# Kernel tuning notes

Measured on AMD Instinct MI355X. Metric: run time of the kernel, lower is better.

## Reference

```python
import jax, jax.numpy as jnp
import numpy as np

B, S, E, H, D = 4, 2048, 1024, 16, 64  # batch, seq, embed, heads, head_dim


def setup_inputs() -> dict:
    key = jax.random.key(0)
    k1, k2, k3 = jax.random.split(key, 3)
    x = jax.random.normal(k1, (B, S, E), dtype=jnp.float32)
    qkv_w = jax.random.normal(k2, (E, H, 3 * D), dtype=jnp.float32) * (1.0 / np.sqrt(E))
    qkv_b = jnp.zeros((H, 3 * D), dtype=jnp.float32)
    out_w = jax.random.normal(k3, (H, D, E), dtype=jnp.float32) * (1.0 / np.sqrt(H * D))
    out_b = jnp.zeros((E,), dtype=jnp.float32)
    return {"x": x, "qkv_w": qkv_w, "qkv_b": qkv_b, "out_w": out_w, "out_b": out_b}


def _large_negative_number(dtype):
    return jnp.asarray(-0.7 * jnp.finfo(dtype).max, dtype=dtype)


def reference(x, qkv_w, qkv_b, out_w, out_b):
    # qkv projection: LinearGeneral(E -> (H, 3D))
    qkv = jnp.einsum('bse,ehd->bshd', x, qkv_w) + qkv_b  # [B,S,H,3D]
    q, k, v = jnp.split(qkv, 3, axis=-1)  # each [B,S,H,D]
    logits = jnp.einsum('bqhd,bkhd->bhqk', q, k)  # [B,H,S,S]
    logits = logits / jnp.sqrt(jnp.asarray(q.shape[-1], logits.dtype))
    mask = jnp.tril(jnp.ones((q.shape[1], q.shape[1]), dtype=jnp.bool_))
    logits = jnp.where(mask, logits, _large_negative_number(logits.dtype))
    probs = jax.nn.softmax(logits, axis=-1)
    attn = jnp.einsum('bhqk,bkhd->bqhd', probs, v)  # [B,S,H,D]
    # output projection: LinearGeneral((H, D) -> E)
    return jnp.einsum('bqhd,hde->bqe', attn, out_w) + out_b
```

## Files before the change

### kernel.cpp

```cpp
#include <hip/hip_runtime.h>

typedef unsigned int u32;
typedef _Float16 f16;
typedef _Float16 f16x8 __attribute__((ext_vector_type(8)));
typedef _Float16 f16x4 __attribute__((ext_vector_type(4)));
typedef float f32x4 __attribute__((ext_vector_type(4)));

#define LOG2E 1.4426950408889634f

__device__ __forceinline__ void gl_lds16(const void* g, void* l) {
  __builtin_amdgcn_global_load_lds(
      (const __attribute__((address_space(1))) u32*)g,
      (__attribute__((address_space(3))) u32*)l, 16, 0, 0);
}

__device__ __forceinline__ f32x4 mfma16(f16x8 a, f16x8 b, f32x4 c) {
  return __builtin_amdgcn_mfma_f32_16x16x32_f16(a, b, c, 0, 0, 0);
}

__global__ void k_cvt(const float* __restrict__ in, f16* __restrict__ out, int n4) {
  int stride = gridDim.x * blockDim.x;
  for (int i = blockIdx.x * blockDim.x + threadIdx.x; i < n4; i += stride) {
    f32x4 v = *(const f32x4*)(in + (size_t)i * 4);
    f16x4 o;
    o[0] = (f16)v[0]; o[1] = (f16)v[1]; o[2] = (f16)v[2]; o[3] = (f16)v[3];
    *(f16x4*)(out + (size_t)i * 4) = o;
  }
}

__global__ void k_tconv(const float* __restrict__ in, f16* __restrict__ out, int R, int C) {
  __shared__ f16 tile[32][33];
  int c0 = blockIdx.x * 32, r0 = blockIdx.y * 32;
  int tx = threadIdx.x, ty = threadIdx.y;
#pragma unroll
  for (int i = ty; i < 32; i += 8)
    tile[i][tx] = (f16)in[(size_t)(r0 + i) * C + c0 + tx];
  __syncthreads();
#pragma unroll
  for (int i = ty; i < 32; i += 8)
    out[(size_t)(c0 + i) * R + r0 + tx] = tile[tx][i];
}


__device__ __forceinline__ void gemm_core(
    const f16* __restrict__ A, const f16* __restrict__ Bt,
    int bm, int bn, f16* SM, int w, int lane, f32x4 (&acc)[4][4]) {
  constexpr int KT = 16;
  const int g = lane >> 4, rl = lane & 15;
  const int l4 = lane >> 2, ls = lane & 3;
  const int wr = w >> 1, wc = w & 1;

  const int cr0 = w * 32 + l4, cr1 = cr0 + 16, br = w * 16 + l4;
  const f16* aS0 = A + (size_t)(bm + cr0) * 1024 + ((ls ^ ((cr0 >> 1) & 3)) * 8);
  const f16* aS1 = A + (size_t)(bm + cr1) * 1024 + ((ls ^ ((cr1 >> 1) & 3)) * 8);
  const f16* bS  = Bt + (size_t)(bn + br) * 1024 + ((ls ^ ((br >> 1) & 3)) * 8);

#define STG_A(b, ks, kt) do { \
    gl_lds16(aS0 + (kt) * 64 + (ks) * 32, SM + (b) * 16384 + (ks) * 8192 + (w * 2 + 0) * 512); \
    gl_lds16(aS1 + (kt) * 64 + (ks) * 32, SM + (b) * 16384 + (ks) * 8192 + (w * 2 + 1) * 512); } while (0)
#define STG_B(b, ks, kt) \
    gl_lds16(bS + (kt) * 64 + (ks) * 32, SM + 49152 + (b) * 8192 + (ks) * 4096 + w * 512)

  STG_A(0, 0, 0); STG_B(0, 0, 0); STG_A(0, 1, 0); STG_B(0, 1, 0);
  STG_A(1, 0, 1); STG_B(1, 0, 1); STG_A(1, 1, 1); STG_B(1, 1, 1);
  asm volatile("s_waitcnt vmcnt(6)" ::: "memory");
  __builtin_amdgcn_s_barrier();

  int c = 0, cs = 2;
#pragma unroll 1
  for (int kt = 0; kt < KT; ++kt) {
    const f16* Ab = SM + c * 16384;
    const f16* Bb = SM + 49152 + c * 8192;
    const bool stg = (kt + 2 < KT);
    f16x8 bf[4][2];

    {
#pragma unroll
      for (int j = 0; j < 4; ++j)
#pragma unroll
        for (int ks = 0; ks < 2; ++ks) {
          const int rb = wc * 64 + j * 16 + rl;
          bf[j][ks] = *(const f16x8*)(Bb + ks * 4096 + rb * 32 + ((g ^ ((rb >> 1) & 3)) * 8));
        }
      f16x8 af[2][2];
#pragma unroll
      for (int mi = 0; mi < 2; ++mi)
#pragma unroll
        for (int ks = 0; ks < 2; ++ks) {
          const int ra = wr * 64 + mi * 16 + rl;
          af[mi][ks] = *(const f16x8*)(Ab + ks * 8192 + ra * 32 + ((g ^ ((ra >> 1) & 3)) * 8));
        }
      if (stg) { STG_A(cs, 0, kt + 2); STG_B(cs, 0, kt + 2); }
      __builtin_amdgcn_s_barrier();
      asm volatile("s_waitcnt lgkmcnt(0)" ::: "memory");
      __builtin_amdgcn_sched_barrier(0);
      __builtin_amdgcn_s_setprio(1);
#pragma unroll
      for (int mi = 0; mi < 2; ++mi)
#pragma unroll
        for (int j = 0; j < 4; ++j) {
          acc[mi][j] = mfma16(af[mi][0], bf[j][0], acc[mi][j]);
          acc[mi][j] = mfma16(af[mi][1], bf[j][1], acc[mi][j]);
        }
      __builtin_amdgcn_s_setprio(0);
      __builtin_amdgcn_sched_barrier(0);
      __builtin_amdgcn_s_barrier();
    }

    {
      f16x8 af[2][2];
#pragma unroll
      for (int mi = 0; mi < 2; ++mi)
#pragma unroll
        for (int ks = 0; ks < 2; ++ks) {
          const int ra = wr * 64 + (2 + mi) * 16 + rl;
          af[mi][ks] = *(const f16x8*)(Ab + ks * 8192 + ra * 32 + ((g ^ ((ra >> 1) & 3)) * 8));
        }
      if (stg) { STG_A(cs, 1, kt + 2); STG_B(cs, 1, kt + 2); }
      __builtin_amdgcn_s_barrier();
      asm volatile("s_waitcnt lgkmcnt(0)" ::: "memory");
      __builtin_amdgcn_sched_barrier(0);
      __builtin_amdgcn_s_setprio(1);
#pragma unroll
      for (int mi = 0; mi < 2; ++mi)
#pragma unroll
        for (int j = 0; j < 4; ++j) {
          acc[2 + mi][j] = mfma16(af[mi][0], bf[j][0], acc[2 + mi][j]);
          acc[2 + mi][j] = mfma16(af[mi][1], bf[j][1], acc[2 + mi][j]);
        }
      __builtin_amdgcn_s_setprio(0);
      __builtin_amdgcn_sched_barrier(0);
      if (kt + 2 < KT)      { asm volatile("s_waitcnt vmcnt(6)" ::: "memory"); }
      else if (kt + 1 < KT) { asm volatile("s_waitcnt vmcnt(0)" ::: "memory"); }
      __builtin_amdgcn_s_barrier();
    }

    c = (c == 2) ? 0 : c + 1;
    cs = (cs == 2) ? 0 : cs + 1;
  }
#undef STG_A
#undef STG_B
}

__global__ __launch_bounds__(512, 2) void k_gemm_qkv3(
    const f16* __restrict__ A, const f16* __restrict__ Bt,
    const float* __restrict__ bias,
    f16* __restrict__ qo, f16* __restrict__ ko2, f16* __restrict__ vto) {
  __shared__ __align__(16) f16 SM[73728];
  const int lin0 = blockIdx.y * 24 + blockIdx.x;
  const int lin = (lin0 & 7) * 96 + (lin0 >> 3);
  const int bn = (lin % 24) * 128, bm = (lin / 24) * 256;
  const int t = threadIdx.x, lane = t & 63, w = t >> 6;
  const int g = lane >> 4, rl = lane & 15;
  const int wr = w >> 1, wc = w & 1;

  f32x4 acc[4][4] = {};
  gemm_core(A, Bt, bm, bn, SM, w, lane, acc);

#pragma unroll
  for (int i = 0; i < 4; ++i)
#pragma unroll
    for (int j = 0; j < 4; ++j)
#pragma unroll
      for (int r = 0; r < 4; ++r) {
        int m = bm + wr * 64 + i * 16 + g * 4 + r;
        int n = bn + wc * 64 + j * 16 + rl;
        float v = acc[i][j][r] + bias[n];
        int b = m >> 11, s = m & 2047;
        int h = n / 192, rem = n - h * 192;
        int tsel = rem >> 6, d = rem & 63;
        size_t bh = (size_t)(b * 16 + h);
        if (tsel == 0)      qo[(bh * 2048 + s) * 64 + d] = (f16)(v * (0.125f * LOG2E));
        else if (tsel == 1) ko2[(bh * 2048 + s) * 64 + d] = (f16)v;
        else                vto[(bh * 64 + d) * 2048 + s] = (f16)v;
      }
}

__global__ __launch_bounds__(512, 2) void k_gemm_out3(
    const f16* __restrict__ A, const f16* __restrict__ Bt,
    const float* __restrict__ bias, float* __restrict__ out) {
  __shared__ __align__(16) f16 SM[73728];
  const int lin0 = blockIdx.y * 8 + blockIdx.x;
  const int lin = (lin0 & 7) * 32 + (lin0 >> 3);
  const int bn = (lin % 8) * 128, bm = (lin / 8) * 256;
  const int t = threadIdx.x, lane = t & 63, w = t >> 6;
  const int g = lane >> 4, rl = lane & 15;
  const int wr = w >> 1, wc = w & 1;

  f32x4 acc[4][4] = {};
  gemm_core(A, Bt, bm, bn, SM, w, lane, acc);

#pragma unroll
  for (int i = 0; i < 4; ++i)
#pragma unroll
    for (int j = 0; j < 4; ++j)
#pragma unroll
      for (int r = 0; r < 4; ++r) {
        int m = bm + wr * 64 + i * 16 + g * 4 + r;
        int n = bn + wc * 64 + j * 16 + rl;
        out[(size_t)m * 1024 + n] = acc[i][j][r] + bias[n];
      }
}

__global__ __launch_bounds__(256, 4) void k_attn2(
    const f16* __restrict__ q, const f16* __restrict__ kgl,
    const f16* __restrict__ vt, f16* __restrict__ o) {
  constexpr int S = 2048;
  __shared__ __align__(16) f16 Ks[2][64 * 64];
  __shared__ __align__(16) f16 Vs[2][64 * 64];
  __shared__ __align__(16) f16 Ps[4][16 * 64];

  const int blk = blockIdx.x;
  const int sidx = blk >> 3;
  const int bh = (blk & 7) * 8 + (sidx & 7);
  const int qb = 15 - (sidx >> 3);

  const int t = threadIdx.x, lane = t & 63, w = t >> 6;
  const int g = lane >> 4, rl = lane & 15;

  const f16* qp = q + ((size_t)bh * S + qb * 128) * 64;
  const f16* kb = kgl + (size_t)bh * S * 64;
  const f16* vb = vt + (size_t)bh * 64 * S;

  f16x8 qf[2][2];
#pragma unroll
  for (int sub = 0; sub < 2; ++sub)
#pragma unroll
    for (int ks = 0; ks < 2; ++ks)
      qf[sub][ks] = *(const f16x8*)(qp + (size_t)(w * 32 + sub * 16 + rl) * 64 + ks * 32 + g * 8);

  f32x4 oacc[2][4] = {};
  float lrow[2] = {0.f, 0.f};

  const int srow = lane >> 3;
  const int sslot = (lane & 7) ^ srow;

  const int nkt = 2 * qb + 2;
  const int qmaxw = qb * 128 + w * 32 + 31;

  auto STAGE = [&](int bufi, int kt) {
#pragma unroll
    for (int i = 0; i < 2; ++i) {
      const int r0 = w * 16 + i * 8;
      gl_lds16(kb + (size_t)(kt * 64 + r0 + srow) * 64 + sslot * 8, &Ks[bufi][r0 * 64]);
      gl_lds16(vb + (size_t)(r0 + srow) * S + kt * 64 + sslot * 8, &Vs[bufi][r0 * 64]);
    }
  };

  STAGE(0, 0);
  __syncthreads();
  int buf = 0;

  for (int kt = 0; kt < nkt; ++kt) {
    if (kt + 1 < nkt) STAGE(buf ^ 1, kt + 1);

    if (kt * 64 <= qmaxw) {
      const f16* Kb = &Ks[buf][0];
      const f16* Vb = &Vs[buf][0];
#pragma unroll
      for (int sub = 0; sub < 2; ++sub) {
        const int qsub = qb * 128 + w * 32 + sub * 16;
        if (kt * 64 > qsub + 15) continue;

        f32x4 sT[4] = {};
#pragma unroll
        for (int j = 0; j < 4; ++j)
#pragma unroll
          for (int ks = 0; ks < 2; ++ks) {
            int row = j * 16 + rl;
            f16x8 kf = *(const f16x8*)(Kb + row * 64 + (((ks * 4 + g) ^ (rl & 7)) * 8));
            sT[j] = mfma16(kf, qf[sub][ks], sT[j]);
          }

        if (kt * 64 + 63 > qsub) {
#pragma unroll
          for (int j = 0; j < 4; ++j)
#pragma unroll
            for (int r = 0; r < 4; ++r)
              if (kt * 64 + j * 16 + g * 4 + r > qsub + rl) sT[j][r] = -1e30f;
        }

        float ps = 0.f;
#pragma unroll
        for (int j = 0; j < 4; ++j) {
          f16x4 pb;
#pragma unroll
          for (int r = 0; r < 4; ++r) {
            float p = exp2f(sT[j][r]);
            ps += p;
            pb[r] = (f16)p;
          }
          *(f16x4*)(&Ps[w][0] + rl * 64 + (((j * 2 + (g >> 1)) ^ (rl & 7)) * 8) + (g & 1) * 4) = pb;
        }
        lrow[sub] += ps;

        asm volatile("s_waitcnt lgkmcnt(0)" ::: "memory");
        __builtin_amdgcn_sched_barrier(0);

        f16x8 pf[2];
#pragma unroll
        for (int ks = 0; ks < 2; ++ks)
          pf[ks] = *(const f16x8*)(&Ps[w][0] + rl * 64 + (((ks * 4 + g) ^ (rl & 7)) * 8));

#pragma unroll
        for (int dj = 0; dj < 4; ++dj)
#pragma unroll
          for (int ks = 0; ks < 2; ++ks) {
            int vrow = dj * 16 + rl;
            f16x8 vf = *(const f16x8*)(Vb + vrow * 64 + (((ks * 4 + g) ^ (rl & 7)) * 8));
            oacc[sub][dj] = mfma16(pf[ks], vf, oacc[sub][dj]);
          }
      }
    }
    __syncthreads();
    buf ^= 1;
  }

  float rinv[2];
#pragma unroll
  for (int sub = 0; sub < 2; ++sub) {
    float s_ = lrow[sub];
    s_ += __shfl_xor(s_, 16, 64);
    s_ += __shfl_xor(s_, 32, 64);
    rinv[sub] = 1.0f / s_;
  }

  const int h = bh & 15;
  const size_t rowb = (size_t)(bh >> 4) * 2048 + qb * 128 + w * 32;
#pragma unroll
  for (int sub = 0; sub < 2; ++sub)
#pragma unroll
    for (int r = 0; r < 4; ++r) {
      float ri = __shfl(rinv[sub], g * 4 + r, 64);
#pragma unroll
      for (int dj = 0; dj < 4; ++dj)
        o[(rowb + sub * 16 + g * 4 + r) * 1024 + h * 64 + dj * 16 + rl] =
            (f16)(oacc[sub][dj][r] * ri);
    }
}

extern "C" void kernel_launch(void* const* d_in, const int* in_sizes, int n_in,
                              void* d_out, int out_size, void* d_ws, size_t ws_size,
                              hipStream_t stream) {
  (void)in_sizes; (void)n_in; (void)out_size; (void)ws_size;
  const float* x    = (const float*)d_in[0];
  const float* wqkv = (const float*)d_in[1];
  const float* bqkv = (const float*)d_in[2];
  const float* wo   = (const float*)d_in[3];
  const float* bo   = (const float*)d_in[4];
  float* out = (float*)d_out;
  char* ws = (char*)d_ws;

  f16* xb    = (f16*)(ws + 0);
  f16* wqkvt = (f16*)(ws + 16777216);
  f16* wot   = (f16*)(ws + 23068672);
  f16* qws   = (f16*)(ws + 25165824);
  f16* kws   = (f16*)(ws + 41943040);
  f16* vtws  = (f16*)(ws + 58720256);
  f16* attnb = xb;

  k_cvt<<<2048, 256, 0, stream>>>(x, xb, 8388608 / 4);
  k_tconv<<<dim3(96, 32), dim3(32, 8), 0, stream>>>(wqkv, wqkvt, 1024, 3072);
  k_tconv<<<dim3(32, 32), dim3(32, 8), 0, stream>>>(wo, wot, 1024, 1024);
  k_gemm_qkv3<<<dim3(24, 32), 512, 0, stream>>>(xb, wqkvt, bqkv, qws, kws, vtws);
  k_attn2<<<1024, 256, 0, stream>>>(qws, kws, vtws, attnb);
  k_gemm_out3<<<dim3(8, 32), 512, 0, stream>>>(attnb, wot, bo, out);
}
```

Before: 203.9 us.

## Restructure projection GEMMs to 4-wave 128x256 tiles with K-step 32

Replaces the 8-wave 256x128 GEMM core with a 4-wave kernel where each wave computes a 128x64 slice (8x4 MFMA accumulators) over K-steps of 32, using a smaller triple-buffered LDS region. The A fragments are shared across all waves and each wave owns a 64-column strip of B, which changes LDS traffic per MFMA and the register footprint. Both QKV and output projection kernels are relaunched with the new tile grid. This risks higher register pressure and fewer waves per CU to hide latency.

```diff
diff --git a/kernel.cpp b/kernel.cpp
--- a/kernel.cpp
+++ b/kernel.cpp
@@ -41,131 +41,116 @@
     out[(size_t)(c0 + i) * R + r0 + tx] = tile[tx][i];
 }
 
-
-__device__ __forceinline__ void gemm_core(
+__device__ __forceinline__ void gemm_fat(
     const f16* __restrict__ A, const f16* __restrict__ Bt,
-    int bm, int bn, f16* SM, int w, int lane, f32x4 (&acc)[4][4]) {
-  constexpr int KT = 16;
+    int bm, int bn, f16* SM, int w, int lane, f32x4 (&acc)[8][4]) {
+  constexpr int KT = 32;
   const int g = lane >> 4, rl = lane & 15;
   const int l4 = lane >> 2, ls = lane & 3;
-  const int wr = w >> 1, wc = w & 1;
-
-  const int cr0 = w * 32 + l4, cr1 = cr0 + 16, br = w * 16 + l4;
-  const f16* aS0 = A + (size_t)(bm + cr0) * 1024 + ((ls ^ ((cr0 >> 1) & 3)) * 8);
-  const f16* aS1 = A + (size_t)(bm + cr1) * 1024 + ((ls ^ ((cr1 >> 1) & 3)) * 8);
-  const f16* bS  = Bt + (size_t)(bn + br) * 1024 + ((ls ^ ((br >> 1) & 3)) * 8);
-
-#define STG_A(b, ks, kt) do { \
-    gl_lds16(aS0 + (kt) * 64 + (ks) * 32, SM + (b) * 16384 + (ks) * 8192 + (w * 2 + 0) * 512); \
-    gl_lds16(aS1 + (kt) * 64 + (ks) * 32, SM + (b) * 16384 + (ks) * 8192 + (w * 2 + 1) * 512); } while (0)
-#define STG_B(b, ks, kt) \
-    gl_lds16(bS + (kt) * 64 + (ks) * 32, SM + 49152 + (b) * 8192 + (ks) * 4096 + w * 512)
-
-  STG_A(0, 0, 0); STG_B(0, 0, 0); STG_A(0, 1, 0); STG_B(0, 1, 0);
-  STG_A(1, 0, 1); STG_B(1, 0, 1); STG_A(1, 1, 1); STG_B(1, 1, 1);
+  const int sslot = ls ^ ((l4 >> 1) & 3);
+
+  const f16* aS = A + (size_t)(bm + w * 32 + l4) * 1024 + sslot * 8;
+  const f16* bS = Bt + (size_t)(bn + w * 16 + l4) * 1024 + sslot * 8;
+  f16* aD = SM + w * 1024;
+  f16* bD = SM + 4096 + w * 512;
+
+#define STGH0(b, kt) do { \
+    gl_lds16(aS + (kt) * 32,          aD + (b) * 12288); \
+    gl_lds16(aS + 16384 + (kt) * 32,  aD + (b) * 12288 + 512); \
+    gl_lds16(bS + (kt) * 32,          bD + (b) * 12288); } while (0)
+#define STGH1(b, kt) do { \
+    gl_lds16(bS + 65536 + (kt) * 32,  bD + (b) * 12288 + 2048); \
+    gl_lds16(bS + 131072 + (kt) * 32, bD + (b) * 12288 + 4096); \
+    gl_lds16(bS + 196608 + (kt) * 32, bD + (b) * 12288 + 6144); } while (0)
+
+  STGH0(0, 0); STGH1(0, 0);
+  STGH0(1, 1); STGH1(1, 1);
   asm volatile("s_waitcnt vmcnt(6)" ::: "memory");
   __builtin_amdgcn_s_barrier();
+
+  const int ro = rl * 32 + ((g ^ ((rl >> 1) & 3)) * 8);
 
   int c = 0, cs = 2;
 #pragma unroll 1
   for (int kt = 0; kt < KT; ++kt) {
-    const f16* Ab = SM + c * 16384;
-    const f16* Bb = SM + 49152 + c * 8192;
+    const f16* SMc = SM + c * 12288;
     const bool stg = (kt + 2 < KT);
-    f16x8 bf[4][2];
+    f16x8 bf[4], af[4];
 
     {
 #pragma unroll
       for (int j = 0; j < 4; ++j)
-#pragma unroll
-        for (int ks = 0; ks < 2; ++ks) {
-          const int rb = wc * 64 + j * 16 + rl;
-          bf[j][ks] = *(const f16x8*)(Bb + ks * 4096 + rb * 32 + ((g ^ ((rb >> 1) & 3)) * 8));
-        }
-      f16x8 af[2][2];
-#pragma unroll
-      for (int mi = 0; mi < 2; ++mi)
-#pragma unroll
-        for (int ks = 0; ks < 2; ++ks) {
-          const int ra = wr * 64 + mi * 16 + rl;
-          af[mi][ks] = *(const f16x8*)(Ab + ks * 8192 + ra * 32 + ((g ^ ((ra >> 1) & 3)) * 8));
-        }
-      if (stg) { STG_A(cs, 0, kt + 2); STG_B(cs, 0, kt + 2); }
+        bf[j] = *(const f16x8*)(SMc + 4096 + w * 2048 + j * 512 + ro);
+#pragma unroll
+      for (int mi = 0; mi < 4; ++mi)
+        af[mi] = *(const f16x8*)(SMc + mi * 512 + ro);
+      if (stg) STGH0(cs, kt + 2);
       __builtin_amdgcn_s_barrier();
       asm volatile("s_waitcnt lgkmcnt(0)" ::: "memory");
       __builtin_amdgcn_sched_barrier(0);
       __builtin_amdgcn_s_setprio(1);
 #pragma unroll
-      for (int mi = 0; mi < 2; ++mi)
-#pragma unroll
-        for (int j = 0; j < 4; ++j) {
-          acc[mi][j] = mfma16(af[mi][0], bf[j][0], acc[mi][j]);
-          acc[mi][j] = mfma16(af[mi][1], bf[j][1], acc[mi][j]);
-        }
+      for (int mi = 0; mi < 4; ++mi)
+#pragma unroll
+        for (int j = 0; j < 4; ++j)
+          acc[mi][j] = mfma16(af[mi], bf[j], acc[mi][j]);
       __builtin_amdgcn_s_setprio(0);
       __builtin_amdgcn_sched_barrier(0);
       __builtin_amdgcn_s_barrier();
     }
 
     {
-      f16x8 af[2][2];
-#pragma unroll
-      for (int mi = 0; mi < 2; ++mi)
-#pragma unroll
-        for (int ks = 0; ks < 2; ++ks) {
-          const int ra = wr * 64 + (2 + mi) * 16 + rl;
-          af[mi][ks] = *(const f16x8*)(Ab + ks * 8192 + ra * 32 + ((g ^ ((ra >> 1) & 3)) * 8));
-        }
-      if (stg) { STG_A(cs, 1, kt + 2); STG_B(cs, 1, kt + 2); }
+#pragma unroll
+      for (int mi = 0; mi < 4; ++mi)
+        af[mi] = *(const f16x8*)(SMc + (4 + mi) * 512 + ro);
+      if (stg) STGH1(cs, kt + 2);
       __builtin_amdgcn_s_barrier();
       asm volatile("s_waitcnt lgkmcnt(0)" ::: "memory");
       __builtin_amdgcn_sched_barrier(0);
       __builtin_amdgcn_s_setprio(1);
 #pragma unroll
-      for (int mi = 0; mi < 2; ++mi)
-#pragma unroll
-        for (int j = 0; j < 4; ++j) {
-          acc[2 + mi][j] = mfma16(af[mi][0], bf[j][0], acc[2 + mi][j]);
-          acc[2 + mi][j] = mfma16(af[mi][1], bf[j][1], acc[2 + mi][j]);
-        }
+      for (int mi = 0; mi < 4; ++mi)
+#pragma unroll
+        for (int j = 0; j < 4; ++j)
+          acc[4 + mi][j] = mfma16(af[mi], bf[j], acc[4 + mi][j]);
       __builtin_amdgcn_s_setprio(0);
       __builtin_amdgcn_sched_barrier(0);
       if (kt + 2 < KT)      { asm volatile("s_waitcnt vmcnt(6)" ::: "memory"); }
       else if (kt + 1 < KT) { asm volatile("s_waitcnt vmcnt(0)" ::: "memory"); }
       __builtin_amdgcn_s_barrier();
+      __builtin_amdgcn_sched_barrier(0);
     }
 
     c = (c == 2) ? 0 : c + 1;
     cs = (cs == 2) ? 0 : cs + 1;
   }
-#undef STG_A
-#undef STG_B
-}
-
-__global__ __launch_bounds__(512, 2) void k_gemm_qkv3(
+#undef STGH0
+#undef STGH1
+}
+
+__global__ __launch_bounds__(256, 2) void k_gemm_qkv4(
     const f16* __restrict__ A, const f16* __restrict__ Bt,
     const float* __restrict__ bias,
     f16* __restrict__ qo, f16* __restrict__ ko2, f16* __restrict__ vto) {
-  __shared__ __align__(16) f16 SM[73728];
-  const int lin0 = blockIdx.y * 24 + blockIdx.x;
+  __shared__ __align__(16) f16 SM[36864];
+  const int lin0 = blockIdx.y * 12 + blockIdx.x;
   const int lin = (lin0 & 7) * 96 + (lin0 >> 3);
-  const int bn = (lin % 24) * 128, bm = (lin / 24) * 256;
+  const int bn = (lin % 12) * 256, bm = (lin / 12) * 128;
   const int t = threadIdx.x, lane = t & 63, w = t >> 6;
   const int g = lane >> 4, rl = lane & 15;
-  const int wr = w >> 1, wc = w & 1;
-
-  f32x4 acc[4][4] = {};
-  gemm_core(A, Bt, bm, bn, SM, w, lane, acc);
-
-#pragma unroll
-  for (int i = 0; i < 4; ++i)
+
+  f32x4 acc[8][4] = {};
+  gemm_fat(A, Bt, bm, bn, SM, w, lane, acc);
+
+#pragma unroll
+  for (int mi = 0; mi < 8; ++mi)
 #pragma unroll
     for (int j = 0; j < 4; ++j)
 #pragma unroll
       for (int r = 0; r < 4; ++r) {
-        int m = bm + wr * 64 + i * 16 + g * 4 + r;
-        int n = bn + wc * 64 + j * 16 + rl;
-        float v = acc[i][j][r] + bias[n];
+        int m = bm + mi * 16 + g * 4 + r;
+        int n = bn + w * 64 + j * 16 + rl;
+        float v = acc[mi][j][r] + bias[n];
         int b = m >> 11, s = m & 2047;
         int h = n / 192, rem = n - h * 192;
         int tsel = rem >> 6, d = rem & 63;
@@ -176,29 +161,28 @@
       }
 }
 
-__global__ __launch_bounds__(512, 2) void k_gemm_out3(
+__global__ __launch_bounds__(256, 2) void k_gemm_out4(
     const f16* __restrict__ A, const f16* __restrict__ Bt,
     const float* __restrict__ bias, float* __restrict__ out) {
-  __shared__ __align__(16) f16 SM[73728];
-  const int lin0 = blockIdx.y * 8 + blockIdx.x;
+  __shared__ __align__(16) f16 SM[36864];
+  const int lin0 = blockIdx.y * 4 + blockIdx.x;
   const int lin = (lin0 & 7) * 32 + (lin0 >> 3);
-  const int bn = (lin % 8) * 128, bm = (lin / 8) * 256;
+  const int bn = (lin % 4) * 256, bm = (lin / 4) * 128;
   const int t = threadIdx.x, lane = t & 63, w = t >> 6;
   const int g = lane >> 4, rl = lane & 15;
-  const int wr = w >> 1, wc = w & 1;
-
-  f32x4 acc[4][4] = {};
-  gemm_core(A, Bt, bm, bn, SM, w, lane, acc);
-
-#pragma unroll
-  for (int i = 0; i < 4; ++i)
+
+  f32x4 acc[8][4] = {};
+  gemm_fat(A, Bt, bm, bn, SM, w, lane, acc);
+
+#pragma unroll
+  for (int mi = 0; mi < 8; ++mi)
 #pragma unroll
     for (int j = 0; j < 4; ++j)
 #pragma unroll
       for (int r = 0; r < 4; ++r) {
-        int m = bm + wr * 64 + i * 16 + g * 4 + r;
-        int n = bn + wc * 64 + j * 16 + rl;
-        out[(size_t)m * 1024 + n] = acc[i][j][r] + bias[n];
+        int m = bm + mi * 16 + g * 4 + r;
+        int n = bn + w * 64 + j * 16 + rl;
+        out[(size_t)m * 1024 + n] = acc[mi][j][r] + bias[n];
       }
 }
 
@@ -362,7 +346,7 @@
   k_cvt<<<2048, 256, 0, stream>>>(x, xb, 8388608 / 4);
   k_tconv<<<dim3(96, 32), dim3(32, 8), 0, stream>>>(wqkv, wqkvt, 1024, 3072);
   k_tconv<<<dim3(32, 32), dim3(32, 8), 0, stream>>>(wo, wot, 1024, 1024);
-  k_gemm_qkv3<<<dim3(24, 32), 512, 0, stream>>>(xb, wqkvt, bqkv, qws, kws, vtws);
+  k_gemm_qkv4<<<dim3(12, 64), 256, 0, stream>>>(xb, wqkvt, bqkv, qws, kws, vtws);
   k_attn2<<<1024, 256, 0, stream>>>(qws, kws, vtws, attnb);
-  k_gemm_out3<<<dim3(8, 32), 512, 0, stream>>>(attnb, wot, bo, out);
-}
+  k_gemm_out4<<<dim3(4, 64), 256, 0, stream>>>(attnb, wot, bo, out);
+}
```

Result: faster. 191.2 us (-6.2%).
